# Performance work log

Hardware: AMD Instinct MI355X
Metric: run time of the kernel (lower is better)

The kernel has to match this reference:

```python
import jax, jax.numpy as jnp
import numpy as np

STRIDE = 1
PAD = 3  # kernel_size // 2 = 7 // 2


def setup_inputs() -> dict:
    key = jax.random.key(0)
    k1, k2, k3 = jax.random.split(key, 3)
    B, Cin, T = 32, 128, 4096
    K, Cout, ks = 4, 256, 7
    x = jax.random.normal(k1, (B, Cin, T), dtype=jnp.float32)
    weight = jax.random.normal(k2, (K, Cout, Cin, ks), dtype=jnp.float32) * 0.01
    bias = jnp.zeros((K, Cout), dtype=jnp.float32)
    rw = jax.random.normal(k3, (K, Cin), dtype=jnp.float32) * 0.05
    rb = jnp.zeros((K,), dtype=jnp.float32)
    return {"x": x, "weight": weight, "bias": bias, "rw": rw, "rb": rb}


def reference(x, weight, bias, rw, rb):
    # x: [B, Cin, T]; weight: [K, Cout, Cin, ks]; bias: [K, Cout]
    K, Cout, Cin, ks = weight.shape
    B = x.shape[0]
    # routing: adaptive avg pool over T -> Linear -> softmax
    pooled = jnp.mean(x, axis=-1)                      # [B, Cin]
    alpha = jax.nn.softmax(pooled @ rw.T + rb, axis=-1)  # [B, K]
    # all K conv branches in one conv by folding K into out-channels
    w_all = weight.reshape(K * Cout, Cin, ks)
    y = jax.lax.conv_general_dilated(
        x, w_all, window_strides=(STRIDE,), padding=[(PAD, PAD)],
        dimension_numbers=("NCH", "OIH", "NCH"))      # [B, K*Cout, T']
    Tp = y.shape[-1]
    y = y.reshape(B, K, Cout, Tp) + bias[None, :, :, None]
    # softmax-routed weighted sum over the K branches
    out = jnp.einsum("bk,bkct->bct", alpha, y)         # [B, Cout, T']
    return out
```

## Files before the change

kernel.cpp:

```cpp
#include <hip/hip_runtime.h>
#include <stdint.h>


#define WEFF_OFF   0u
#define POOLED_OFF 14680064u
#define BEFF_OFF   14696448u

typedef short short8 __attribute__((ext_vector_type(8)));
typedef float f32x16 __attribute__((ext_vector_type(16)));

__device__ __forceinline__ unsigned short f2bf(float f) {
  unsigned int u = __builtin_bit_cast(unsigned int, f);
  u += 0x7fffu + ((u >> 16) & 1u);
  return (unsigned short)(u >> 16);
}

__global__ __launch_bounds__(256) void k_pool(const float* __restrict__ x,
                                              float* __restrict__ pooled) {
  __shared__ float ws4[4];
  int row = blockIdx.x;
  const float* src = x + (size_t)row * 4096 + threadIdx.x * 16;
  float s = 0.f;
  #pragma unroll
  for (int i = 0; i < 4; ++i) {
    float4 v = *(const float4*)(src + i * 4);
    s += (v.x + v.y) + (v.z + v.w);
  }
  #pragma unroll
  for (int off = 32; off > 0; off >>= 1) s += __shfl_down(s, off);
  int lane = threadIdx.x & 63, wv = threadIdx.x >> 6;
  if (lane == 0) ws4[wv] = s;
  __syncthreads();
  if (threadIdx.x == 0) pooled[row] = (ws4[0] + ws4[1]) + (ws4[2] + ws4[3]);
}

__global__ __launch_bounds__(256) void k_fold(
    const float* __restrict__ w, const float* __restrict__ pooled,
    const float* __restrict__ rw, const float* __restrict__ rb,
    const float* __restrict__ bias, unsigned short* __restrict__ weff,
    float* __restrict__ bias_eff) {
  __shared__ float al[32][4];
  int tid = threadIdx.x;
  if (tid < 128) {
    int b = tid >> 2, k = tid & 3;
    const float* pp = pooled + b * 128;
    const float* rwk = rw + k * 128;
    float s = rb[k];
    #pragma unroll 8
    for (int j = 0; j < 128; ++j) s += pp[j] * (1.0f / 4096.0f) * rwk[j];
    al[b][k] = s;
  }
  __syncthreads();
  if (tid < 32) {
    float l0 = al[tid][0], l1 = al[tid][1], l2 = al[tid][2], l3 = al[tid][3];
    float m = fmaxf(fmaxf(l0, l1), fmaxf(l2, l3));
    float e0 = __expf(l0 - m), e1 = __expf(l1 - m);
    float e2 = __expf(l2 - m), e3 = __expf(l3 - m);
    float inv = 1.0f / (e0 + e1 + e2 + e3);
    al[tid][0] = e0 * inv; al[tid][1] = e1 * inv;
    al[tid][2] = e2 * inv; al[tid][3] = e3 * inv;
  }
  __syncthreads();
  if (blockIdx.x == 0) {
    #pragma unroll
    for (int b = 0; b < 32; ++b) {
      float s = 0.f;
      #pragma unroll
      for (int k = 0; k < 4; ++k) s += al[b][k] * bias[k * 256 + tid];
      bias_eff[b * 256 + tid] = s;
    }
  }
  int gid = blockIdx.x * 256 + tid;
  int cb = gid / 14336;
  int r = gid - cb * 14336;
  int step = r >> 8;
  int ct = (r >> 6) & 3;
  int lpos = r & 63;
  int s7 = step >> 3, slice = step & 7;
  int cout = cb * 128 + ct * 32 + (lpos & 31);
  int ci0 = slice * 16 + (lpos >> 5) * 8;
  float wv[4][8];
  #pragma unroll
  for (int k = 0; k < 4; ++k) {
    const float* src = w + ((size_t)(k * 256 + cout) * 128 + ci0) * 7 + s7;
    #pragma unroll
    for (int j = 0; j < 8; ++j) wv[k][j] = src[j * 7];
  }
  unsigned short* dst = weff + (size_t)gid * 8;
  #pragma unroll 4
  for (int b = 0; b < 32; ++b) {
    float a0 = al[b][0], a1 = al[b][1], a2 = al[b][2], a3 = al[b][3];
    unsigned short h[8];
    #pragma unroll
    for (int j = 0; j < 8; ++j)
      h[j] = f2bf(a0 * wv[0][j] + a1 * wv[1][j] + a2 * wv[2][j] + a3 * wv[3][j]);
    uint4 o;
    o.x = (unsigned)h[0] | ((unsigned)h[1] << 16);
    o.y = (unsigned)h[2] | ((unsigned)h[3] << 16);
    o.z = (unsigned)h[4] | ((unsigned)h[5] << 16);
    o.w = (unsigned)h[6] | ((unsigned)h[7] << 16);
    *(uint4*)(dst + (size_t)b * 229376) = o;
  }
}

__global__ __launch_bounds__(256, 2) void k_conv3(
    const float* __restrict__ x, const unsigned short* __restrict__ weff,
    const float* __restrict__ bias_eff, float* __restrict__ out) {
  __shared__ __align__(16) unsigned short xs[16 * 262 * 8];
  int phys = blockIdx.x;
  int logical = (phys & 7) * 64 + (phys >> 3);
  int b = logical >> 4, tb = logical & 15;
  int tid = threadIdx.x;
  int t00 = tb << 8;

  {
    const float* xbase = x + (size_t)b * 128 * 4096;
    int xrow = t00 - 3 + tid;
    bool valid = (unsigned)xrow < 4096u;
    #pragma unroll
    for (int g = 0; g < 16; ++g) {
      float f[8];
      #pragma unroll
      for (int u = 0; u < 8; ++u)
        f[u] = valid ? xbase[(size_t)(g * 8 + u) * 4096 + xrow] : 0.f;
      uint4 o;
      o.x = (unsigned)f2bf(f[0]) | ((unsigned)f2bf(f[1]) << 16);
      o.y = (unsigned)f2bf(f[2]) | ((unsigned)f2bf(f[3]) << 16);
      o.z = (unsigned)f2bf(f[4]) | ((unsigned)f2bf(f[5]) << 16);
      o.w = (unsigned)f2bf(f[6]) | ((unsigned)f2bf(f[7]) << 16);
      *(uint4*)(&xs[(g * 262 + tid) * 8]) = o;
    }
    if (tid < 128) {
      int g = tid >> 3, r8 = tid & 7;
      if (r8 < 6) {
        int row2 = 256 + r8;
        int xrow2 = t00 - 3 + row2;
        bool v2 = (unsigned)xrow2 < 4096u;
        float f[8];
        #pragma unroll
        for (int u = 0; u < 8; ++u)
          f[u] = v2 ? xbase[(size_t)(g * 8 + u) * 4096 + xrow2] : 0.f;
        uint4 o;
        o.x = (unsigned)f2bf(f[0]) | ((unsigned)f2bf(f[1]) << 16);
        o.y = (unsigned)f2bf(f[2]) | ((unsigned)f2bf(f[3]) << 16);
        o.z = (unsigned)f2bf(f[4]) | ((unsigned)f2bf(f[5]) << 16);
        o.w = (unsigned)f2bf(f[6]) | ((unsigned)f2bf(f[7]) << 16);
        *(uint4*)(&xs[(g * 262 + row2) * 8]) = o;
      }
    }
  }
  __syncthreads();

  int wave = tid >> 6, lane = tid & 63;
  int l31 = lane & 31, lhi = lane >> 5;
  int wm = wave & 1, wn = wave >> 1;
  const short8* wb8 = (const short8*)weff + (size_t)b * 28672 + lane;

  for (int cb = 0; cb < 2; ++cb) {
    f32x16 acc[2][4];
    #pragma unroll
    for (int mi = 0; mi < 2; ++mi)
      #pragma unroll
      for (int ni = 0; ni < 4; ++ni)
        acc[mi][ni] = (f32x16)(0.f);

    const short8* wfrag = wb8 + (size_t)cb * 14336 + (wm * 2) * 64;
    short8 av[2];
    #pragma unroll
    for (int mi = 0; mi < 2; ++mi) av[mi] = wfrag[mi * 64];

    #pragma unroll 2
    for (int step = 0; step < 56; ++step) {
      int s = step >> 3, slice = step & 7;
      short8 avn[2];
      if (step < 55) {
        #pragma unroll
        for (int mi = 0; mi < 2; ++mi)
          avn[mi] = wfrag[(step + 1) * 256 + mi * 64];
      }
      short8 bv[4];
      int prow = (slice * 2 + lhi) * 262 + s;
      #pragma unroll
      for (int ni = 0; ni < 4; ++ni) {
        int tt = wn * 128 + ni * 32 + l31;
        bv[ni] = *(const short8*)(&xs[(size_t)(prow + tt) * 8]);
      }
      #pragma unroll
      for (int mi = 0; mi < 2; ++mi)
        #pragma unroll
        for (int ni = 0; ni < 4; ++ni)
          acc[mi][ni] = __builtin_amdgcn_mfma_f32_32x32x16_bf16(
              av[mi], bv[ni], acc[mi][ni], 0, 0, 0);
      #pragma unroll
      for (int mi = 0; mi < 2; ++mi) av[mi] = avn[mi];
    }

    int crow0 = b * 256 + cb * 128;
    #pragma unroll
    for (int mi = 0; mi < 2; ++mi) {
      #pragma unroll
      for (int r = 0; r < 16; ++r) {
        int c = wm * 64 + mi * 32 + (r & 3) + 8 * (r >> 2) + 4 * lhi;
        float bb = bias_eff[crow0 + c];
        float* orow = out + (size_t)(crow0 + c) * 4096 + t00;
        #pragma unroll
        for (int ni = 0; ni < 4; ++ni)
          orow[wn * 128 + ni * 32 + l31] = acc[mi][ni][r] + bb;
      }
    }
  }
}

extern "C" void kernel_launch(void* const* d_in, const int* in_sizes, int n_in,
                              void* d_out, int out_size, void* d_ws, size_t ws_size,
                              hipStream_t stream) {
  const float* x    = (const float*)d_in[0];
  const float* w    = (const float*)d_in[1];
  const float* bias = (const float*)d_in[2];
  const float* rw   = (const float*)d_in[3];
  const float* rb   = (const float*)d_in[4];
  float* out = (float*)d_out;
  char* ws = (char*)d_ws;
  unsigned short* weff = (unsigned short*)(ws + WEFF_OFF);
  float* pooled        = (float*)(ws + POOLED_OFF);
  float* bias_eff      = (float*)(ws + BEFF_OFF);

  hipLaunchKernelGGL(k_pool,  dim3(4096), dim3(256), 0, stream, x, pooled);
  hipLaunchKernelGGL(k_fold,  dim3(112),  dim3(256), 0, stream,
                     w, pooled, rw, rb, bias, weff, bias_eff);
  hipLaunchKernelGGL(k_conv3, dim3(512),  dim3(256), 0, stream,
                     x, weff, bias_eff, out);
}
```

Baseline: 248.9 us.

## Split fold across more blocks and deepen weight prefetch in conv kernel

The fold kernel now launches four times as many blocks, each handling 8 batches instead of 32, to spread weight-folding work across more CUs. The conv kernel's weight fragment loads now use a double-buffered scheme that prefetches 4 steps of weights at a time, fully unrolled, instead of one step ahead. This is meant to hide global-load latency behind the MFMA work. It raises register pressure and code size, and every fold block recomputes the routing softmax and re-reads its weight slice.

```diff
diff --git a/kernel.cpp b/kernel.cpp
--- a/kernel.cpp
+++ b/kernel.cpp
@@ -70,9 +70,10 @@
       bias_eff[b * 256 + tid] = s;
     }
   }
-  int gid = blockIdx.x * 256 + tid;
-  int cb = gid / 14336;
-  int r = gid - cb * 14336;
+  int bq = blockIdx.x & 3;
+  int pos = (blockIdx.x >> 2) * 256 + tid;
+  int cb = pos / 14336;
+  int r = pos - cb * 14336;
   int step = r >> 8;
   int ct = (r >> 6) & 3;
   int lpos = r & 63;
@@ -86,9 +87,10 @@
     #pragma unroll
     for (int j = 0; j < 8; ++j) wv[k][j] = src[j * 7];
   }
-  unsigned short* dst = weff + (size_t)gid * 8;
-  #pragma unroll 4
-  for (int b = 0; b < 32; ++b) {
+  unsigned short* dst = weff + (size_t)pos * 8;
+  #pragma unroll
+  for (int bi = 0; bi < 8; ++bi) {
+    int b = bq * 8 + bi;
     float a0 = al[b][0], a1 = al[b][1], a2 = al[b][2], a3 = al[b][3];
     unsigned short h[8];
     #pragma unroll
@@ -103,7 +105,7 @@
   }
 }
 
-__global__ __launch_bounds__(256, 2) void k_conv3(
+__global__ __launch_bounds__(256, 2) void k_conv5(
     const float* __restrict__ x, const unsigned short* __restrict__ weff,
     const float* __restrict__ bias_eff, float* __restrict__ out) {
   __shared__ __align__(16) unsigned short xs[16 * 262 * 8];
@@ -164,36 +166,47 @@
       for (int ni = 0; ni < 4; ++ni)
         acc[mi][ni] = (f32x16)(0.f);
 
-    const short8* wfrag = wb8 + (size_t)cb * 14336 + (wm * 2) * 64;
-    short8 av[2];
-    #pragma unroll
-    for (int mi = 0; mi < 2; ++mi) av[mi] = wfrag[mi * 64];
-
-    #pragma unroll 2
-    for (int step = 0; step < 56; ++step) {
-      int s = step >> 3, slice = step & 7;
-      short8 avn[2];
-      if (step < 55) {
-        #pragma unroll
-        for (int mi = 0; mi < 2; ++mi)
-          avn[mi] = wfrag[(step + 1) * 256 + mi * 64];
+    const short8* wf = wb8 + (size_t)cb * 14336 + (wm * 2) * 64;
+    short8 wA[2][4], wB[2][4];
+
+    #define PREF(BUF, hg)                                            \
+      _Pragma("unroll")                                              \
+      for (int mi = 0; mi < 2; ++mi)                                 \
+        _Pragma("unroll")                                            \
+        for (int sl = 0; sl < 4; ++sl)                               \
+          BUF[mi][sl] = wf[((hg) * 4 + sl) * 256 + mi * 64];
+
+    #define COMP(BUF, hg)                                            \
+      _Pragma("unroll")                                              \
+      for (int sl = 0; sl < 4; ++sl) {                               \
+        int step = (hg) * 4 + sl;                                    \
+        int s = step >> 3, slice = step & 7;                         \
+        int prow = (slice * 2 + lhi) * 262 + s;                      \
+        short8 bv[4];                                                \
+        _Pragma("unroll")                                            \
+        for (int ni = 0; ni < 4; ++ni) {                             \
+          int tt = wn * 128 + ni * 32 + l31;                         \
+          bv[ni] = *(const short8*)(&xs[(size_t)(prow + tt) * 8]);   \
+        }                                                            \
+        _Pragma("unroll")                                            \
+        for (int mi = 0; mi < 2; ++mi)                               \
+          _Pragma("unroll")                                          \
+          for (int ni = 0; ni < 4; ++ni)                             \
+            acc[mi][ni] = __builtin_amdgcn_mfma_f32_32x32x16_bf16(   \
+                BUF[mi][sl], bv[ni], acc[mi][ni], 0, 0, 0);          \
       }
-      short8 bv[4];
-      int prow = (slice * 2 + lhi) * 262 + s;
-      #pragma unroll
-      for (int ni = 0; ni < 4; ++ni) {
-        int tt = wn * 128 + ni * 32 + l31;
-        bv[ni] = *(const short8*)(&xs[(size_t)(prow + tt) * 8]);
-      }
-      #pragma unroll
-      for (int mi = 0; mi < 2; ++mi)
-        #pragma unroll
-        for (int ni = 0; ni < 4; ++ni)
-          acc[mi][ni] = __builtin_amdgcn_mfma_f32_32x32x16_bf16(
-              av[mi], bv[ni], acc[mi][ni], 0, 0, 0);
-      #pragma unroll
-      for (int mi = 0; mi < 2; ++mi) av[mi] = avn[mi];
-    }
+
+    PREF(wA, 0);
+    #pragma unroll
+    for (int hg2 = 0; hg2 < 7; ++hg2) {
+      int hg = hg2 * 2;
+      PREF(wB, hg + 1);
+      COMP(wA, hg);
+      if (hg2 < 6) { PREF(wA, hg + 2); }
+      COMP(wB, hg + 1);
+    }
+    #undef PREF
+    #undef COMP
 
     int crow0 = b * 256 + cb * 128;
     #pragma unroll
@@ -226,8 +239,8 @@
   float* bias_eff      = (float*)(ws + BEFF_OFF);
 
   hipLaunchKernelGGL(k_pool,  dim3(4096), dim3(256), 0, stream, x, pooled);
-  hipLaunchKernelGGL(k_fold,  dim3(112),  dim3(256), 0, stream,
+  hipLaunchKernelGGL(k_fold,  dim3(448),  dim3(256), 0, stream,
                      w, pooled, rw, rb, bias, weff, bias_eff);
-  hipLaunchKernelGGL(k_conv3, dim3(512),  dim3(256), 0, stream,
+  hipLaunchKernelGGL(k_conv5, dim3(512),  dim3(256), 0, stream,
                      x, weff, bias_eff, out);
 }
```

After: 253.8 us. About the same (+2.0%).
